# Kernel tuning notes

Hardware: AMD Instinct MI355X
Metric: run time of the kernel (lower is better)

## Reference

```python
import jax, jax.numpy as jnp
import numpy as np
import math

K = 3          # kernel_size
P_GEM = 3.0    # GeM power
EPS_GEM = 1e-6
EPS_NORM = 1e-12


def _l2n(x, axis):
    n = jnp.sqrt(jnp.sum(x * x, axis=axis, keepdims=True))
    return x / jnp.maximum(n, EPS_NORM)


def setup_inputs() -> dict:
    key = jax.random.key(0)
    ks = jax.random.split(key, 7)
    b, hw, c, nc = 32, 196, 768, 4096
    hidden = c  # mlp_ratio = 1
    return {
        "patch_tokens": jax.random.normal(ks[0], (b, hw, c), dtype=jnp.float32),
        "fc1_w": jax.random.normal(ks[1], (c, hidden), dtype=jnp.float32) * 0.02,
        "fc1_b": jnp.zeros((hidden,), dtype=jnp.float32),
        "fc2_w": jax.random.normal(ks[2], (hidden, c), dtype=jnp.float32) * 0.02,
        "fc2_b": jnp.zeros((c,), dtype=jnp.float32),
        "head_w": jax.random.normal(ks[3], (c, nc), dtype=jnp.float32) * 0.02,
        "head_b": jnp.zeros((nc,), dtype=jnp.float32),
    }


def reference(patch_tokens, fc1_w, fc1_b, fc2_w, fc2_b, head_w, head_b):
    b, hw, c = patch_tokens.shape
    h = w = int(math.sqrt(hw))

    # ---- SpaceSelfAware: pad -> unfold (3x3 local windows) -> multiply ----
    img = jnp.transpose(patch_tokens, (0, 2, 1)).reshape(b, c, h, w)
    # ZeroPad2d((left=1, right=1, top=2, bottom=0)) for kernel_size=3
    padded = jnp.pad(img, ((0, 0), (0, 0), (K - 1, 0), (K // 2, K // 2)))
    # stack the 9 shifted views, row-major over (ki, kj) matching nn.Unfold
    wins = jnp.stack(
        [padded[:, :, ki:ki + h, kj:kj + w] for ki in range(K) for kj in range(K)],
        axis=2,
    )  # (b, c, 9, h, w)
    y = wins.reshape(b, c, K, K, hw)
    y = jnp.transpose(y, (0, 4, 1, 2, 3))  # (b, hw, c, K, K)
    ssa = patch_tokens[:, :, :, None, None] * y  # (b, hw, c, K, K)

    # ---- space_fusion: L2Norm(dim=1) then GeM(p=3) over the KxK window ----
    ssa = _l2n(ssa, axis=1)
    pooled = jnp.mean(jnp.clip(ssa, EPS_GEM, None) ** P_GEM, axis=(-2, -1)) ** (1.0 / P_GEM)  # (b, hw, c)

    # ---- residual + L2 normalize over channels + Mlp ----
    tokens = pooled + patch_tokens
    tokens = _l2n(tokens, axis=-1)
    hdn = jax.nn.gelu(tokens @ fc1_w + fc1_b, approximate=False)
    tokens = hdn @ fc2_w + fc2_b  # (b, hw, c)

    # ---- GeMHead: GeM(p=3) over tokens, linear to nc, L2 normalize ----
    g = jnp.mean(jnp.clip(tokens, EPS_GEM, None) ** P_GEM, axis=1) ** (1.0 / P_GEM)  # (b, c)
    desc = g @ head_w + head_b  # (b, nc)
    desc = _l2n(desc, axis=-1)
    return desc
```

## Files before the change

### kernel.cpp

```cpp
#include <hip/hip_runtime.h>
#include <hip/hip_bf16.h>
#include <math.h>

#define B   32
#define P   196
#define C   768
#define NC  4096
#define HH  14
#define KSPLIT 12
#define NT  12
#define M6  6272
#define TW  (768 * 32)
#define TM  (M6 * 32)

typedef _Float16 half8 __attribute__((ext_vector_type(8)));
typedef _Float16 half4 __attribute__((ext_vector_type(4)));
typedef float f32x4 __attribute__((ext_vector_type(4)));

#define GLOAD_LDS16(g, l)                                                      \
    __builtin_amdgcn_global_load_lds(                                          \
        (const __attribute__((address_space(1))) void*)(g),                    \
        (__attribute__((address_space(3))) void*)(l), 16, 0, 0)

__global__ __launch_bounds__(256) void k_ssa(const float* __restrict__ t,
                                             _Float16* __restrict__ outP,
                                             float* __restrict__ partial) {
    const int b = blockIdx.y, cb = blockIdx.x, c0 = cb * 16;
    __shared__ float xp_[256 * 16];
    __shared__ float part[4][9][16];
    __shared__ float inv_norm[9][16];
    __shared__ _Float16 outT[P][16];
    const int tid = threadIdx.x;
    const int cc = tid & 15, g = tid >> 4, wv = tid >> 6;

#pragma unroll
    for (int q = 0; q < 16; ++q) xp_[q * 256 + tid] = 0.0f;
    __syncthreads();

    for (int idx = tid; idx < 784; idx += 256) {
        const int p = idx >> 2, c = (idx & 3) * 4;
        const int i = p / HH, j = p % HH;
        *(float4*)&xp_[((i + 2) * 16 + (j + 1)) * 16 + c] =
            *(const float4*)&t[((size_t)b * P + p) * C + c0 + c];
    }
    __syncthreads();

    float s[9] = {};
    {
        int i = 0, j = g;
        if (j >= HH) { j -= HH; i = 1; }
        for (int p = g; p < P; p += 16) {
            const int base = ((i + 2) * 16 + (j + 1)) * 16 + cc;
            const float xp = xp_[base];
            const float xp2 = xp * xp;
#pragma unroll
            for (int k = 0; k < 9; ++k) {
                const int off = ((k / 3) - 2) * 16 + (k % 3) - 1;
                const float nb = xp_[base + off * 16];
                s[k] += xp2 * nb * nb;
            }
            j += 2; ++i;
            if (j >= HH) { j -= HH; ++i; }
        }
    }
#pragma unroll
    for (int k = 0; k < 9; ++k) {
        float r = s[k];
        r += __shfl_xor(r, 16);
        r += __shfl_xor(r, 32);
        s[k] = r;
    }
    if ((tid & 63) < 16) {
#pragma unroll
        for (int k = 0; k < 9; ++k) part[wv][k][cc] = s[k];
    }
    __syncthreads();
    if (tid < 144) {
        const int k = tid >> 4, c2 = tid & 15;
        const float t4 = part[0][k][c2] + part[1][k][c2] +
                         part[2][k][c2] + part[3][k][c2];
        inv_norm[k][c2] = 1.0f / fmaxf(sqrtf(t4), 1e-12f);
    }
    __syncthreads();

    float invn[9];
#pragma unroll
    for (int k = 0; k < 9; ++k) invn[k] = inv_norm[k][cc];

    {
        int i = 0, j = g;
        if (j >= HH) { j -= HH; i = 1; }
        for (int p = g; p < P; p += 16) {
            const int base = ((i + 2) * 16 + (j + 1)) * 16 + cc;
            const float xp = xp_[base];
            float acc = 0.0f;
#pragma unroll
            for (int k = 0; k < 9; ++k) {
                const int off = ((k / 3) - 2) * 16 + (k % 3) - 1;
                const float v = xp * xp_[base + off * 16];
                const float u = fmaxf(v * invn[k], 1e-6f);
                acc += u * u * u;
            }
            const float val = cbrtf(acc * (1.0f / 9.0f)) + xp;
            float rs = val * val;
            rs += __shfl_xor(rs, 1);
            rs += __shfl_xor(rs, 2);
            rs += __shfl_xor(rs, 4);
            rs += __shfl_xor(rs, 8);
            outT[p][cc] = (_Float16)val;
            if (cc == 0) partial[(size_t)cb * M6 + b * P + p] = rs;
            j += 2; ++i;
            if (j >= HH) { j -= HH; ++i; }
        }
    }
    __syncthreads();
    const int kb = cb >> 1, kbase = (cb & 1) * 16;
    for (int idx = tid; idx < P * 2; idx += 256) {
        const int p = idx >> 1, h = idx & 1;
        const half8 v = *(const half8*)&outT[p][h * 8];
        const int row = b * P + p;
        const int slot = ((kbase + h * 8) >> 3) ^ ((row >> 1) & 3);
        *(half8*)&outP[(size_t)kb * TM + (size_t)row * 32 + slot * 8] = v;
    }
}

__global__ __launch_bounds__(256) void k_prep(const float* __restrict__ W1,
                                              const float* __restrict__ W2,
                                              _Float16* __restrict__ O1,
                                              _Float16* __restrict__ O2,
                                              const float* __restrict__ spart,
                                              float* __restrict__ invv) {
    if (blockIdx.z == 2) {
        const int row = (blockIdx.y * 24 + blockIdx.x) * 256 + threadIdx.x;
        if (row < M6) {
            float s = 0.0f;
#pragma unroll 8
            for (int cb = 0; cb < 48; ++cb) s += spart[(size_t)cb * M6 + row];
            invv[row] = 1.0f / fmaxf(sqrtf(s), 1e-12f);
        }
        return;
    }
    const float* W = blockIdx.z ? W2 : W1;
    _Float16* WtP = blockIdx.z ? O2 : O1;
    __shared__ float tt[32][33];
    const int k0 = blockIdx.x * 32, n0 = blockIdx.y * 32;
    const int r = threadIdx.x / 32, c = threadIdx.x % 32;
#pragma unroll
    for (int q = 0; q < 4; ++q)
        tt[r + q * 8][c] = W[(size_t)(k0 + r + q * 8) * C + n0 + c];
    __syncthreads();
    const int nl = threadIdx.x >> 3, h = threadIdx.x & 7;
    const int n = n0 + nl;
    half4 v;
#pragma unroll
    for (int j = 0; j < 4; ++j) v[j] = (_Float16)tt[h * 4 + j][nl];
    const int el = (h * 4) ^ (((n >> 1) & 3) << 3);
    *(half4*)&WtP[(size_t)blockIdx.x * TW + (size_t)n * 32 + el] = v;
}

template <bool GELU>
__global__ __launch_bounds__(256) void k_mfma_gemm(
    const _Float16* __restrict__ TokP,
    const _Float16* __restrict__ WtP,
    const float* __restrict__ bias,
    const float* __restrict__ invv,
    _Float16* __restrict__ Cout,
    float* __restrict__ gpart) {
    __shared__ _Float16 lA[3][2][64][32];
    __shared__ _Float16 lB[3][2][64][32];
    __shared__ float part2[2][2][64];
    const int tid = threadIdx.x;
    const int w = tid >> 6, l = tid & 63;
    const int l15 = l & 15, lk = l >> 4;

    const int lid = blockIdx.x;
    int vm, vn;
    if (lid < 1152) { vm = (lid / 96) * 8 + (lid & 7); vn = (lid % 96) >> 3; }
    else            { const int r = lid - 1152; vm = 96 + r / 12; vn = r % 12; }
    const int m0 = vm * 64, n0 = vn * 64;
    const int wn = (w & 1) * 32, wm = (w >> 1) * 32;

    f32x4 acc[2][2] = {};

    const int kbsel = w & 1;
    const bool isB = (w >= 2);
    const _Float16* srcBase =
        isB ? (TokP + (size_t)m0 * 32) : (WtP + (size_t)n0 * 32);
    const size_t tileStride = isB ? (size_t)TM : (size_t)TW;
    _Float16* dst0 = isB ? &lB[0][kbsel][0][0] : &lA[0][kbsel][0][0];

#define ISSUE(tt, bf_)                                                         \
    {   const _Float16* s_ = srcBase + (size_t)(2 * (tt) + kbsel) * tileStride;\
        _Float16* d_ = dst0 + (size_t)(bf_) * 4096;                            \
        GLOAD_LDS16(s_ + l * 8,        d_ + l * 8);                            \
        GLOAD_LDS16(s_ + 512 + l * 8,  d_ + 512 + l * 8);                      \
        GLOAD_LDS16(s_ + 1024 + l * 8, d_ + 1024 + l * 8);                     \
        GLOAD_LDS16(s_ + 1536 + l * 8, d_ + 1536 + l * 8); }

    ISSUE(0, 0); ISSUE(1, 1); ISSUE(2, 2);

    for (int t = 0; t < NT; ++t) {
        if (t < NT - 2)       asm volatile("s_waitcnt vmcnt(8)" ::: "memory");
        else if (t == NT - 2) asm volatile("s_waitcnt vmcnt(4)" ::: "memory");
        else                  asm volatile("s_waitcnt vmcnt(0)" ::: "memory");
        __builtin_amdgcn_s_barrier();
        __builtin_amdgcn_sched_barrier(0);

        const int buf = t % 3;
#pragma unroll
        for (int kk = 0; kk < 2; ++kk) {
            half8 af[2], bf[2];
#pragma unroll
            for (int fa = 0; fa < 2; ++fa) {
                const int rowA = wn + fa * 16 + l15;
                const int colA = (lk ^ ((rowA >> 1) & 3)) * 8;
                af[fa] = *(const half8*)&lA[buf][kk][rowA][colA];
            }
#pragma unroll
            for (int fb = 0; fb < 2; ++fb) {
                const int rowB = wm + fb * 16 + l15;
                const int colB = (lk ^ ((rowB >> 1) & 3)) * 8;
                bf[fb] = *(const half8*)&lB[buf][kk][rowB][colB];
            }
#pragma unroll
            for (int fa = 0; fa < 2; ++fa)
#pragma unroll
                for (int fb = 0; fb < 2; ++fb)
                    acc[fa][fb] = __builtin_amdgcn_mfma_f32_16x16x32_f16(
                        af[fa], bf[fb], acc[fa][fb], 0, 0, 0);
        }
        asm volatile("s_waitcnt lgkmcnt(0)" ::: "memory");
        __builtin_amdgcn_s_barrier();
        __builtin_amdgcn_sched_barrier(0);
        if (t < NT - 3) ISSUE(t + 3, buf);
    }
#undef ISSUE

    const int b0 = m0 / P;
    const int rsplit = (b0 + 1) * P;
    float invm[2];
    if constexpr (GELU) {
#pragma unroll
        for (int fb = 0; fb < 2; ++fb)
            invm[fb] = invv[m0 + wm + fb * 16 + l15];
    }
#pragma unroll
    for (int fa = 0; fa < 2; ++fa) {
        const int nb = n0 + wn + fa * 16 + lk * 4;
        const float4 bv = *(const float4*)&bias[nb];
        if constexpr (GELU) {
#pragma unroll
            for (int fb = 0; fb < 2; ++fb) {
                const int m = m0 + wm + fb * 16 + l15;
                half4 o;
#pragma unroll
                for (int rr = 0; rr < 4; ++rr) {
                    float v = acc[fa][fb][rr] * invm[fb] + ((const float*)&bv)[rr];
                    v = 0.5f * v * (1.0f + erff(v * 0.70710678118654752f));
                    o[rr] = (_Float16)v;
                }
                const int el = (nb & 31) ^ (((m >> 1) & 3) << 3);
                *(half4*)&Cout[(size_t)(nb >> 5) * TM + (size_t)m * 32 + el] = o;
            }
        } else {
#pragma unroll
            for (int rr = 0; rr < 4; ++rr) {
                float s0 = 0.0f, s1 = 0.0f;
#pragma unroll
                for (int fb = 0; fb < 2; ++fb) {
                    const int m = m0 + wm + fb * 16 + l15;
                    const float v = acc[fa][fb][rr] + ((const float*)&bv)[rr];
                    const float u = fmaxf(v, 1e-6f);
                    const float u3 = u * u * u;
                    if (m >= rsplit) s1 += u3; else s0 += u3;
                }
                s0 += __shfl_xor(s0, 1); s0 += __shfl_xor(s0, 2);
                s0 += __shfl_xor(s0, 4); s0 += __shfl_xor(s0, 8);
                s1 += __shfl_xor(s1, 1); s1 += __shfl_xor(s1, 2);
                s1 += __shfl_xor(s1, 4); s1 += __shfl_xor(s1, 8);
                if (l15 == 0) {
                    part2[w >> 1][0][wn + fa * 16 + lk * 4 + rr] = s0;
                    part2[w >> 1][1][wn + fa * 16 + lk * 4 + rr] = s1;
                }
            }
        }
    }
    if constexpr (!GELU) {
        __syncthreads();
        if (tid < 128) {
            const int seg = tid >> 6, nn = tid & 63;
            const float tot = part2[0][seg][nn] + part2[1][seg][nn];
            if (seg == 0) {
                const int q = vm - ((b0 * 49) >> 4);
                gpart[((size_t)b0 * 4 + q) * C + n0 + nn] = tot;
            } else if (rsplit < m0 + 64) {
                gpart[((size_t)(b0 + 1) * 4 + 0) * C + n0 + nn] = tot;
            }
        }
    }
}

__global__ __launch_bounds__(256) void k_head1(const float* __restrict__ gpart,
                                               const float* __restrict__ W,
                                               float* __restrict__ partial) {
    const int n0 = blockIdx.x * 64;
    const int k0 = blockIdx.y * 64;
    __shared__ float gs[32][64];
    __shared__ float part[4][32][64];
    const int tid = threadIdx.x;

    for (int idx = tid; idx < 32 * 64; idx += 256) {
        const int b = idx >> 6, kk = idx & 63;
        const float* gp = &gpart[((size_t)b * 4) * C + k0 + kk];
        const float s = gp[0] + gp[C] + gp[2 * C] + gp[3 * C];
        gs[b][kk] = cbrtf(s * (1.0f / (float)P));
    }
    __syncthreads();

    const int c = tid & 63, q = tid >> 6;
    float acc[32] = {};
#pragma unroll
    for (int kk = 0; kk < 16; ++kk) {
        const int k = q * 16 + kk;
        const float wv = W[(size_t)(k0 + k) * NC + n0 + c];
#pragma unroll
        for (int b = 0; b < 32; ++b) acc[b] += gs[b][k] * wv;
    }
#pragma unroll
    for (int b = 0; b < 32; ++b) part[q][b][c] = acc[b];
    __syncthreads();

    for (int o = tid; o < 32 * 64; o += 256) {
        const int b = o >> 6, cc = o & 63;
        const float v = part[0][b][cc] + part[1][b][cc] +
                        part[2][b][cc] + part[3][b][cc];
        partial[((size_t)blockIdx.y * 32 + b) * NC + n0 + cc] = v;
    }
}

__global__ __launch_bounds__(256) void k_head2(const float* __restrict__ partial,
                                               const float* __restrict__ hb,
                                               float* __restrict__ out) {
    const int n = blockIdx.x * 256 + threadIdx.x;
    const int b = blockIdx.y;
    float s = hb[n];
#pragma unroll
    for (int ks = 0; ks < KSPLIT; ++ks)
        s += partial[((size_t)ks * 32 + b) * NC + n];
    out[(size_t)b * NC + n] = s;
}

__global__ __launch_bounds__(256) void k_outnorm(float* __restrict__ out) {
    const int b = blockIdx.x;
    float* r = out + (size_t)b * NC;
    const int tid = threadIdx.x;
    float v[16];
    float s = 0.0f;
#pragma unroll
    for (int q = 0; q < 16; ++q) {
        v[q] = r[tid + q * 256];
        s += v[q] * v[q];
    }
    __shared__ float partial[4];
    __shared__ float inv;
#pragma unroll
    for (int off = 32; off > 0; off >>= 1) s += __shfl_xor(s, off);
    if ((tid & 63) == 0) partial[tid >> 6] = s;
    __syncthreads();
    if (tid == 0)
        inv = 1.0f / fmaxf(sqrtf(partial[0] + partial[1] + partial[2] + partial[3]), 1e-12f);
    __syncthreads();
#pragma unroll
    for (int q = 0; q < 16; ++q) r[tid + q * 256] = v[q] * inv;
}

extern "C" void kernel_launch(void* const* d_in, const int* in_sizes, int n_in,
                              void* d_out, int out_size, void* d_ws, size_t ws_size,
                              hipStream_t stream) {
    const float* patch  = (const float*)d_in[0];
    const float* fc1_w  = (const float*)d_in[1];
    const float* fc1_b  = (const float*)d_in[2];
    const float* fc2_w  = (const float*)d_in[3];
    const float* fc2_b  = (const float*)d_in[4];
    const float* head_w = (const float*)d_in[5];
    const float* head_b = (const float*)d_in[6];
    float* out = (float*)d_out;

    const size_t big = (size_t)B * P * C;
    _Float16* tokU  = (_Float16*)d_ws;
    _Float16* hdnP  = tokU + big;
    _Float16* wt1   = hdnP + big;
    _Float16* wt2   = wt1 + C * C;
    float*    spart = (float*)(wt2 + C * C);
    float*    invv  = spart + 48 * (size_t)M6;
    float*    gpart = invv + M6;
    float*    hpart = gpart + (size_t)B * 4 * C;

    k_ssa<<<dim3(48, B), dim3(256), 0, stream>>>(patch, tokU, spart);
    k_prep<<<dim3(C / 32, C / 32, 3), dim3(256), 0, stream>>>(
        fc1_w, fc2_w, wt1, wt2, spart, invv);
    k_mfma_gemm<true><<<dim3(1176), dim3(256), 0, stream>>>(
        tokU, wt1, fc1_b, invv, hdnP, nullptr);
    k_mfma_gemm<false><<<dim3(1176), dim3(256), 0, stream>>>(
        hdnP, wt2, fc2_b, nullptr, nullptr, gpart);
    k_head1<<<dim3(NC / 64, KSPLIT), dim3(256), 0, stream>>>(
        gpart, head_w, hpart);
    k_head2<<<dim3(NC / 256, B), dim3(256), 0, stream>>>(hpart, head_b, out);
    k_outnorm<<<dim3(B), dim3(256), 0, stream>>>(out);
}
```

Baseline: 82.90 us.

## Fold weight prep into SSA kernel and inverse-norm reduction into GEMM1 prologue

The weight transpose/convert work moves into extra blocks of the SSA launch (z=1), and the per-row inverse-norm reduction over 48 channel-block partials is computed inside each GEMM1 block into shared memory. This removes the separate k_prep launch and the invv global round trip. In exchange each GEMM1 block serially sums 48 strided partials before its main loop, with an added barrier, and the grid doubles with many early-exiting blocks.

Result: no change. 82.01 us (-1.1%).

```diff
diff --git a/kernel.cpp b/kernel.cpp
--- a/kernel.cpp
+++ b/kernel.cpp
@@ -24,13 +24,43 @@
 
 __global__ __launch_bounds__(256) void k_ssa(const float* __restrict__ t,
                                              _Float16* __restrict__ outP,
-                                             float* __restrict__ partial) {
-    const int b = blockIdx.y, cb = blockIdx.x, c0 = cb * 16;
+                                             float* __restrict__ spart,
+                                             const float* __restrict__ W1,
+                                             const float* __restrict__ W2,
+                                             _Float16* __restrict__ O1,
+                                             _Float16* __restrict__ O2) {
     __shared__ float xp_[256 * 16];
     __shared__ float part[4][9][16];
     __shared__ float inv_norm[9][16];
     __shared__ _Float16 outT[P][16];
     const int tid = threadIdx.x;
+
+    if (blockIdx.z == 1) {
+        const int idx = blockIdx.y * 48 + blockIdx.x;
+        if (idx >= 1152) return;
+        const bool second = idx >= 576;
+        const int id2 = second ? idx - 576 : idx;
+        const float* W = second ? W2 : W1;
+        _Float16* WtP = second ? O2 : O1;
+        const int kb = id2 / 24, nb2 = id2 % 24;
+        const int k0 = kb * 32, n0 = nb2 * 32;
+        float (*tt)[33] = (float (*)[33])xp_;
+        const int r = tid / 32, c = tid % 32;
+#pragma unroll
+        for (int q = 0; q < 4; ++q)
+            tt[r + q * 8][c] = W[(size_t)(k0 + r + q * 8) * C + n0 + c];
+        __syncthreads();
+        const int nl = tid >> 3, h = tid & 7;
+        const int n = n0 + nl;
+        half4 v;
+#pragma unroll
+        for (int j = 0; j < 4; ++j) v[j] = (_Float16)tt[h * 4 + j][nl];
+        const int el = (h * 4) ^ (((n >> 1) & 3) << 3);
+        *(half4*)&WtP[(size_t)kb * TW + (size_t)n * 32 + el] = v;
+        return;
+    }
+
+    const int b = blockIdx.y, cb = blockIdx.x, c0 = cb * 16;
     const int cc = tid & 15, g = tid >> 4, wv = tid >> 6;
 
 #pragma unroll
@@ -108,7 +138,7 @@
             rs += __shfl_xor(rs, 4);
             rs += __shfl_xor(rs, 8);
             outT[p][cc] = (_Float16)val;
-            if (cc == 0) partial[(size_t)cb * M6 + b * P + p] = rs;
+            if (cc == 0) spart[(size_t)cb * M6 + b * P + p] = rs;
             j += 2; ++i;
             if (j >= HH) { j -= HH; ++i; }
         }
@@ -124,51 +154,18 @@
     }
 }
 
-__global__ __launch_bounds__(256) void k_prep(const float* __restrict__ W1,
-                                              const float* __restrict__ W2,
-                                              _Float16* __restrict__ O1,
-                                              _Float16* __restrict__ O2,
-                                              const float* __restrict__ spart,
-                                              float* __restrict__ invv) {
-    if (blockIdx.z == 2) {
-        const int row = (blockIdx.y * 24 + blockIdx.x) * 256 + threadIdx.x;
-        if (row < M6) {
-            float s = 0.0f;
-#pragma unroll 8
-            for (int cb = 0; cb < 48; ++cb) s += spart[(size_t)cb * M6 + row];
-            invv[row] = 1.0f / fmaxf(sqrtf(s), 1e-12f);
-        }
-        return;
-    }
-    const float* W = blockIdx.z ? W2 : W1;
-    _Float16* WtP = blockIdx.z ? O2 : O1;
-    __shared__ float tt[32][33];
-    const int k0 = blockIdx.x * 32, n0 = blockIdx.y * 32;
-    const int r = threadIdx.x / 32, c = threadIdx.x % 32;
-#pragma unroll
-    for (int q = 0; q < 4; ++q)
-        tt[r + q * 8][c] = W[(size_t)(k0 + r + q * 8) * C + n0 + c];
-    __syncthreads();
-    const int nl = threadIdx.x >> 3, h = threadIdx.x & 7;
-    const int n = n0 + nl;
-    half4 v;
-#pragma unroll
-    for (int j = 0; j < 4; ++j) v[j] = (_Float16)tt[h * 4 + j][nl];
-    const int el = (h * 4) ^ (((n >> 1) & 3) << 3);
-    *(half4*)&WtP[(size_t)blockIdx.x * TW + (size_t)n * 32 + el] = v;
-}
-
 template <bool GELU>
 __global__ __launch_bounds__(256) void k_mfma_gemm(
     const _Float16* __restrict__ TokP,
     const _Float16* __restrict__ WtP,
     const float* __restrict__ bias,
-    const float* __restrict__ invv,
+    const float* __restrict__ spart,
     _Float16* __restrict__ Cout,
     float* __restrict__ gpart) {
     __shared__ _Float16 lA[3][2][64][32];
     __shared__ _Float16 lB[3][2][64][32];
     __shared__ float part2[2][2][64];
+    __shared__ float invS[64];
     const int tid = threadIdx.x;
     const int w = tid >> 6, l = tid & 63;
     const int l15 = l & 15, lk = l >> 4;
@@ -179,6 +176,17 @@
     else            { const int r = lid - 1152; vm = 96 + r / 12; vn = r % 12; }
     const int m0 = vm * 64, n0 = vn * 64;
     const int wn = (w & 1) * 32, wm = (w >> 1) * 32;
+
+    if constexpr (GELU) {
+        if (tid < 64) {
+            float s = 0.0f;
+#pragma unroll 8
+            for (int cb = 0; cb < 48; ++cb)
+                s += spart[(size_t)cb * M6 + m0 + tid];
+            invS[tid] = 1.0f / fmaxf(sqrtf(s), 1e-12f);
+        }
+        __syncthreads();
+    }
 
     f32x4 acc[2][2] = {};
 
@@ -242,7 +250,7 @@
     if constexpr (GELU) {
 #pragma unroll
         for (int fb = 0; fb < 2; ++fb)
-            invm[fb] = invv[m0 + wm + fb * 16 + l15];
+            invm[fb] = invS[wm + fb * 16 + l15];
     }
 #pragma unroll
     for (int fa = 0; fa < 2; ++fa) {
@@ -392,15 +400,13 @@
     _Float16* wt1   = hdnP + big;
     _Float16* wt2   = wt1 + C * C;
     float*    spart = (float*)(wt2 + C * C);
-    float*    invv  = spart + 48 * (size_t)M6;
-    float*    gpart = invv + M6;
+    float*    gpart = spart + 48 * (size_t)M6;
     float*    hpart = gpart + (size_t)B * 4 * C;
 
-    k_ssa<<<dim3(48, B), dim3(256), 0, stream>>>(patch, tokU, spart);
-    k_prep<<<dim3(C / 32, C / 32, 3), dim3(256), 0, stream>>>(
-        fc1_w, fc2_w, wt1, wt2, spart, invv);
+    k_ssa<<<dim3(48, B, 2), dim3(256), 0, stream>>>(
+        patch, tokU, spart, fc1_w, fc2_w, wt1, wt2);
     k_mfma_gemm<true><<<dim3(1176), dim3(256), 0, stream>>>(
-        tokU, wt1, fc1_b, invv, hdnP, nullptr);
+        tokU, wt1, fc1_b, spart, hdnP, nullptr);
     k_mfma_gemm<false><<<dim3(1176), dim3(256), 0, stream>>>(
         hdnP, wt2, fc2_b, nullptr, nullptr, gpart);
     k_head1<<<dim3(NC / 64, KSPLIT), dim3(256), 0, stream>>>(
```
